# Kernel optimization log

Hardware: AMD Instinct MI355X
Metric: run time of the kernel (lower is better)

Reference implementation:

```python
import jax, jax.numpy as jnp
import numpy as np

B, D_IN, UNITS, KFEAT = 2048, 2048, 1024, 49


def setup_inputs() -> dict:
    key = jax.random.key(0)
    ks = jax.random.split(key, 10)
    s = 0.02  # small init scale to keep sigmoids/tanh unsaturated
    return {
        "inputs": jax.random.normal(ks[0], (B, D_IN), jnp.float32),
        "h_tm": jax.random.normal(ks[1], (B, UNITS), jnp.float32),
        "m_tm": jax.random.normal(ks[2], (B, UNITS), jnp.float32),
        "v_seq": jax.random.normal(ks[3], (B, KFEAT, UNITS), jnp.float32),
        # gate weights stacked along output dim in order [f, i, o, g, a]
        "W_gates": jax.random.normal(ks[4], (UNITS, 5 * UNITS), jnp.float32) * s,
        "U_gates": jax.random.normal(ks[5], (D_IN, 5 * UNITS), jnp.float32) * s,
        "b_gates": jnp.zeros((5 * UNITS,), jnp.float32),
        "W_z": jax.random.normal(ks[6], (UNITS, KFEAT + 1), jnp.float32) * s,
        "U_z": jax.random.normal(ks[7], (UNITS, KFEAT + 1), jnp.float32) * s,
        "W_h": jax.random.normal(ks[8], (KFEAT + 1, 1), jnp.float32) * s,
    }


def reference(inputs, h_tm, m_tm, v_seq, W_gates, U_gates, b_gates, W_z, U_z, W_h):
    U = h_tm.shape[-1]
    # fused gate pre-activations: [B, 5U]
    z = h_tm @ W_gates + inputs @ U_gates + b_gates
    f, i, o, g, a = (z[:, j * U:(j + 1) * U] for j in range(5))
    ft = jax.nn.sigmoid(f)
    it = jax.nn.sigmoid(i)
    ot = jax.nn.sigmoid(o)
    gt = jax.nn.sigmoid(g)
    at = jnp.tanh(a)
    mt = m_tm * ft + it * at               # memory cell
    tanh_mt = jnp.tanh(mt)
    ht = ot * tanh_mt                      # hidden state
    st = gt * tanh_mt                      # visual sentinel
    # sentinel-augmented features: [B, K+1, U]
    v_expand = jnp.concatenate([v_seq, st[:, None, :]], axis=1)
    vtt = jnp.einsum('bku,uz->bkz', v_expand, W_z)   # [B, K+1, K+1]
    dtt = (ht @ U_z)[:, None, :]                     # broadcast over K+1 (K.repeat)
    zt = jnp.einsum('bkz,zo->bko', jnp.tanh(vtt + dtt), W_h)  # [B, K+1, 1]
    # NOTE: original uses keras softmax with default axis=-1 on a size-1 axis
    alpha_t = jax.nn.softmax(zt, axis=-1)            # [B, K+1, 1]
    ct = jnp.sum(alpha_t * v_expand, axis=1)         # batch_dot(axes=1) + squeeze
    return (ht + ct, ht, mt)
```

## Files before the change

kernel.cpp:

```cpp
#include <hip/hip_runtime.h>
#include <stdint.h>

#define BB   2048
#define DIN  2048
#define UU   1024
#define KF   49
#define GM   2048
#define GK   3072
#define GN   5120

typedef __bf16  bf16x8 __attribute__((ext_vector_type(8)));
typedef float   f32x4  __attribute__((ext_vector_type(4)));

static __device__ __forceinline__ unsigned short f2bf(float f) {
    union { float f; unsigned u; } x; x.f = f;
    unsigned u = x.u;
    unsigned r = (u + 0x7fffu + ((u >> 16) & 1u)) >> 16;
    return (unsigned short)r;
}

__global__ void prep(const float* __restrict__ h, const float* __restrict__ x,
                     const float* __restrict__ Wg, const float* __restrict__ Ug,
                     unsigned short* __restrict__ A, unsigned short* __restrict__ Wt) {
    __shared__ float t[32][36];
    if (blockIdx.x < 6144) {
        int idx = blockIdx.x * 256 + threadIdx.x;
        int b = idx / (GK / 4);
        int k = (idx % (GK / 4)) * 4;
        float4 v;
        if (k < UU) v = *(const float4*)(h + (size_t)b * UU + k);
        else        v = *(const float4*)(x + (size_t)b * DIN + (k - UU));
        ushort4 o;
        o.x = f2bf(v.x); o.y = f2bf(v.y); o.z = f2bf(v.z); o.w = f2bf(v.w);
        *(ushort4*)(A + (size_t)idx * 4) = o;
    } else {
        int bid2 = blockIdx.x - 6144;
        int k0 = (bid2 % (GK / 32)) * 32;
        int n0 = (bid2 / (GK / 32)) * 32;
        int r  = threadIdx.x >> 3;
        int cq = threadIdx.x & 7;
        int k = k0 + r;
        const float* src = (k < UU) ? (Wg + (size_t)k * GN) : (Ug + (size_t)(k - UU) * GN);
        *(float4*)&t[r][cq * 4] = *(const float4*)(src + n0 + cq * 4);
        __syncthreads();
        ushort4 o;
        o.x = f2bf(t[cq * 4 + 0][r]);
        o.y = f2bf(t[cq * 4 + 1][r]);
        o.z = f2bf(t[cq * 4 + 2][r]);
        o.w = f2bf(t[cq * 4 + 3][r]);
        *(ushort4*)(Wt + (size_t)(n0 + r) * GK + k0 + cq * 4) = o;
    }
}

__global__ __launch_bounds__(256, 2) void gemm_fused(
        const unsigned short* __restrict__ A, const unsigned short* __restrict__ Wt,
        const float* __restrict__ m_tm, const float* __restrict__ bg,
        const float* __restrict__ v_seq, float* __restrict__ out) {
    __shared__ __align__(16) char lds[18432];

    const int tid  = threadIdx.x;
    const int lane = tid & 63;
    const int wave = tid >> 6;
    const int wr = wave >> 1, wc = wave & 1;
    const int brow  = blockIdx.y * 128;
    const int ucol0 = blockIdx.x * 32;

    f32x4 acc[4][5];
#pragma unroll
    for (int m = 0; m < 4; m++)
#pragma unroll
        for (int g = 0; g < 5; g++) acc[m][g] = (f32x4){0.f, 0.f, 0.f, 0.f};

    const unsigned short* src[5];
    int ldsoff[5];
    bool valid[5];
#pragma unroll
    for (int t = 0; t < 5; t++) {
        int base = t * 256 + wave * 64;
        int j = base + lane;
        valid[t]  = (base < 1152);
        ldsoff[t] = j * 16;
        if (j < 512) {
            src[t] = A + (size_t)(brow + (j >> 2)) * GK + (j & 3) * 8;
        } else {
            int j2 = j - 512;
            int g = j2 >> 7;
            int n = (j2 >> 2) & 31;
            int c = j2 & 3;
            int gg = (g > 4) ? 4 : g;
            src[t] = Wt + ((size_t)gg * UU + ucol0 + n) * GK + c * 8;
        }
    }

    float4 vacc[4];
#pragma unroll
    for (int r = 0; r < 4; r++) vacc[r] = (float4){0.f, 0.f, 0.f, 0.f};
    const float* vp = v_seq + ((size_t)(brow + (tid >> 3)) * KF) * UU + ucol0 + (tid & 7) * 4;

    for (int k0 = 0; k0 < GK; k0 += 32) {
#pragma unroll
        for (int t = 0; t < 5; t++)
            if (valid[t])
                __builtin_amdgcn_global_load_lds(
                    (const __attribute__((address_space(1))) void*)(src[t] + k0),
                    (__attribute__((address_space(3))) void*)(lds + ldsoff[t]), 16, 0, 0);

        {
            const int kk = k0 >> 6;
            const float4 va0 = *(const float4*)(vp + ((size_t)0  * KF + kk) * UU);
            const float4 va1 = *(const float4*)(vp + ((size_t)32 * KF + kk) * UU);
            const float4 vb0 = *(const float4*)(vp + ((size_t)64 * KF + kk) * UU);
            const float4 vb1 = *(const float4*)(vp + ((size_t)96 * KF + kk) * UU);
            if (((k0 >> 5) & 1) == 0) {
                vacc[0].x += va0.x; vacc[0].y += va0.y; vacc[0].z += va0.z; vacc[0].w += va0.w;
                vacc[1].x += va1.x; vacc[1].y += va1.y; vacc[1].z += va1.z; vacc[1].w += va1.w;
            } else {
                vacc[2].x += vb0.x; vacc[2].y += vb0.y; vacc[2].z += vb0.z; vacc[2].w += vb0.w;
                vacc[3].x += vb1.x; vacc[3].y += vb1.y; vacc[3].z += vb1.z; vacc[3].w += vb1.w;
            }
        }

        __syncthreads();

        bf16x8 af[4], bfg[5];
#pragma unroll
        for (int m = 0; m < 4; m++)
            af[m] = *(const bf16x8*)(lds + (wr * 64 + m * 16 + (lane & 15)) * 64 + (lane >> 4) * 16);
#pragma unroll
        for (int g = 0; g < 5; g++)
            bfg[g] = *(const bf16x8*)(lds + 8192 + g * 2048 + (wc * 16 + (lane & 15)) * 64 + (lane >> 4) * 16);
#pragma unroll
        for (int m = 0; m < 4; m++)
#pragma unroll
            for (int g = 0; g < 5; g++)
                acc[m][g] = __builtin_amdgcn_mfma_f32_16x16x32_bf16(af[m], bfg[g], acc[m][g], 0, 0, 0);
        __syncthreads();
    }

#pragma unroll
    for (int r = 0; r < 4; r++) {
        const float4 v = *(const float4*)(vp + ((size_t)(32 * r) * KF + 48) * UU);
        vacc[r].x += v.x; vacc[r].y += v.y; vacc[r].z += v.z; vacc[r].w += v.w;
    }

    float* lv = (float*)lds;
    {
        const int lr = tid >> 3, lc = (tid & 7) * 4;
#pragma unroll
        for (int r = 0; r < 4; r++)
            *(float4*)&lv[(size_t)(lr + 32 * r) * 36 + lc] = vacc[r];
    }
    __syncthreads();

    const int ucol = ucol0 + wc * 16 + (lane & 15);
    const int lcol = wc * 16 + (lane & 15);
    const float b0 = bg[0 * UU + ucol];
    const float b1 = bg[1 * UU + ucol];
    const float b2 = bg[2 * UU + ucol];
    const float b3 = bg[3 * UU + ucol];
    const float b4 = bg[4 * UU + ucol];
    const int r0 = brow + wr * 64 + ((lane >> 4) << 2);
    const int lr0 = wr * 64 + ((lane >> 4) << 2);
    float* out0 = out;
    float* out1 = out + (size_t)GM * UU;
    float* out2 = out + 2 * (size_t)GM * UU;
#pragma unroll
    for (int m = 0; m < 4; m++) {
#pragma unroll
        for (int j = 0; j < 4; j++) {
            const int row = r0 + m * 16 + j;
            const size_t idx = (size_t)row * UU + ucol;
            const float vs  = lv[(size_t)(lr0 + m * 16 + j) * 36 + lcol];
            const float mtm = m_tm[idx];
            const float f = acc[m][0][j] + b0;
            const float i = acc[m][1][j] + b1;
            const float o = acc[m][2][j] + b2;
            const float g = acc[m][3][j] + b3;
            const float a = acc[m][4][j] + b4;
            const float ft = 1.f / (1.f + __expf(-f));
            const float it = 1.f / (1.f + __expf(-i));
            const float ot = 1.f / (1.f + __expf(-o));
            const float gt = 1.f / (1.f + __expf(-g));
            const float at = tanhf(a);
            const float mtv = mtm * ft + it * at;
            const float tm  = tanhf(mtv);
            const float ht  = ot * tm;
            const float st  = gt * tm;
            out0[idx] = ht + vs + st;
            out1[idx] = ht;
            out2[idx] = mtv;
        }
    }
}

extern "C" void kernel_launch(void* const* d_in, const int* in_sizes, int n_in,
                              void* d_out, int out_size, void* d_ws, size_t ws_size,
                              hipStream_t stream) {
    (void)in_sizes; (void)n_in; (void)out_size; (void)ws_size;
    const float* inputs  = (const float*)d_in[0];
    const float* h_tm    = (const float*)d_in[1];
    const float* m_tm    = (const float*)d_in[2];
    const float* v_seq   = (const float*)d_in[3];
    const float* W_gates = (const float*)d_in[4];
    const float* U_gates = (const float*)d_in[5];
    const float* b_gates = (const float*)d_in[6];

    char* ws = (char*)d_ws;
    unsigned short* Abf = (unsigned short*)ws;
    unsigned short* Wt  = (unsigned short*)(ws + 12582912);
    float* out = (float*)d_out;

    hipLaunchKernelGGL(prep, dim3(6144 + (GK / 32) * (GN / 32)), dim3(256), 0, stream,
                       h_tm, inputs, W_gates, U_gates, Abf, Wt);
    hipLaunchKernelGGL(gemm_fused, dim3(UU / 32, GM / 128), dim3(256), 0, stream,
                       Abf, Wt, m_tm, b_gates, v_seq, out);
}
```

Before: 209.3 us.

## Double-buffer LDS staging, widen block to 64 units with 8 waves, interleave gate weights

The fused GEMM kernel now uses 512 threads covering 64 output units per block and double-buffers the LDS tiles, so global-to-LDS loads for the next K step overlap MFMA work on the current one and one barrier per step is dropped. The prep kernel writes the transposed weights with the five gates interleaved per unit, which makes each block's B tile one contiguous slab. The v_seq reduction is re-indexed to the wider tile. In exchange the kernel uses more LDS (56 KB per block), which may reduce occupancy, and halves the number of blocks.

```diff
diff --git a/kernel.cpp b/kernel.cpp
--- a/kernel.cpp
+++ b/kernel.cpp
@@ -8,6 +8,13 @@
 #define GM   2048
 #define GK   3072
 #define GN   5120
+
+#define BM    128
+#define UC    64
+#define BROWS 320
+#define BKS   32
+#define NST   96
+#define BUFB  28672
 
 typedef __bf16  bf16x8 __attribute__((ext_vector_type(8)));
 typedef float   f32x4  __attribute__((ext_vector_type(4)));
@@ -43,27 +50,31 @@
         const float* src = (k < UU) ? (Wg + (size_t)k * GN) : (Ug + (size_t)(k - UU) * GN);
         *(float4*)&t[r][cq * 4] = *(const float4*)(src + n0 + cq * 4);
         __syncthreads();
+        int n = n0 + r;
+        int u = n & (UU - 1);
+        int g = n >> 10;
         ushort4 o;
         o.x = f2bf(t[cq * 4 + 0][r]);
         o.y = f2bf(t[cq * 4 + 1][r]);
         o.z = f2bf(t[cq * 4 + 2][r]);
         o.w = f2bf(t[cq * 4 + 3][r]);
-        *(ushort4*)(Wt + (size_t)(n0 + r) * GK + k0 + cq * 4) = o;
-    }
-}
-
-__global__ __launch_bounds__(256, 2) void gemm_fused(
+        *(ushort4*)(Wt + (size_t)(u * 5 + g) * GK + k0 + cq * 4) = o;
+    }
+}
+
+__global__ __launch_bounds__(512, 2) void gemm_fused(
         const unsigned short* __restrict__ A, const unsigned short* __restrict__ Wt,
         const float* __restrict__ m_tm, const float* __restrict__ bg,
         const float* __restrict__ v_seq, float* __restrict__ out) {
-    __shared__ __align__(16) char lds[18432];
+    __shared__ __align__(16) char lds[2 * 28672];
 
     const int tid  = threadIdx.x;
     const int lane = tid & 63;
     const int wave = tid >> 6;
-    const int wr = wave >> 1, wc = wave & 1;
-    const int brow  = blockIdx.y * 128;
-    const int ucol0 = blockIdx.x * 32;
+    const int wr = wave >> 2;
+    const int wc = wave & 3;
+    const int brow  = blockIdx.y * BM;
+    const int ucol0 = blockIdx.x * UC;
 
     f32x4 acc[4][5];
 #pragma unroll
@@ -71,84 +82,97 @@
 #pragma unroll
         for (int g = 0; g < 5; g++) acc[m][g] = (f32x4){0.f, 0.f, 0.f, 0.f};
 
-    const unsigned short* src[5];
-    int ldsoff[5];
-    bool valid[5];
-#pragma unroll
-    for (int t = 0; t < 5; t++) {
-        int base = t * 256 + wave * 64;
-        int j = base + lane;
-        valid[t]  = (base < 1152);
-        ldsoff[t] = j * 16;
+    const unsigned short* src[4];
+    int ldsoff[4];
+#pragma unroll
+    for (int t = 0; t < 4; t++) {
+        int j = t * 512 + tid;
         if (j < 512) {
             src[t] = A + (size_t)(brow + (j >> 2)) * GK + (j & 3) * 8;
+            ldsoff[t] = j * 16;
         } else {
-            int j2 = j - 512;
-            int g = j2 >> 7;
-            int n = (j2 >> 2) & 31;
-            int c = j2 & 3;
-            int gg = (g > 4) ? 4 : g;
-            src[t] = Wt + ((size_t)gg * UU + ucol0 + n) * GK + c * 8;
-        }
-    }
-
-    float4 vacc[4];
-#pragma unroll
-    for (int r = 0; r < 4; r++) vacc[r] = (float4){0.f, 0.f, 0.f, 0.f};
-    const float* vp = v_seq + ((size_t)(brow + (tid >> 3)) * KF) * UU + ucol0 + (tid & 7) * 4;
-
-    for (int k0 = 0; k0 < GK; k0 += 32) {
-#pragma unroll
-        for (int t = 0; t < 5; t++)
-            if (valid[t])
-                __builtin_amdgcn_global_load_lds(
-                    (const __attribute__((address_space(1))) void*)(src[t] + k0),
-                    (__attribute__((address_space(3))) void*)(lds + ldsoff[t]), 16, 0, 0);
-
+            int jj = j - 512;
+            if (jj > 1279) jj = 1279;
+            src[t] = Wt + (size_t)((size_t)ucol0 * 5 + (jj >> 2)) * GK + (jj & 3) * 8;
+            ldsoff[t] = 8192 + jj * 16;
+        }
+    }
+
+    const int aoff = (wr * 64 + (lane & 15)) * 64 + (lane >> 4) * 16;
+    const int boff = 8192 + ((wc * 16 + (lane & 15)) * 5) * 64 + (lane >> 4) * 16;
+
+    auto STAGE = [&](int kstep, int bufbase) {
+        const int koff = kstep * BKS;
+#pragma unroll
+        for (int t = 0; t < 3; t++)
+            __builtin_amdgcn_global_load_lds(
+                (const __attribute__((address_space(1))) void*)(src[t] + koff),
+                (__attribute__((address_space(3))) void*)(lds + bufbase + ldsoff[t]), 16, 0, 0);
+        if (tid < 256)
+            __builtin_amdgcn_global_load_lds(
+                (const __attribute__((address_space(1))) void*)(src[3] + koff),
+                (__attribute__((address_space(3))) void*)(lds + bufbase + ldsoff[3]), 16, 0, 0);
+    };
+
+    auto COMPUTE = [&](int bufbase) {
+        bf16x8 af[4], bfr[5];
+#pragma unroll
+        for (int m = 0; m < 4; m++) af[m]  = *(const bf16x8*)(lds + bufbase + aoff + m * 1024);
+#pragma unroll
+        for (int g = 0; g < 5; g++) bfr[g] = *(const bf16x8*)(lds + bufbase + boff + g * 64);
+#pragma unroll
+        for (int m = 0; m < 4; m++)
+#pragma unroll
+            for (int g = 0; g < 5; g++)
+                acc[m][g] = __builtin_amdgcn_mfma_f32_16x16x32_bf16(af[m], bfr[g], acc[m][g], 0, 0, 0);
+    };
+
+    const float* vp = v_seq + (size_t)(brow + (tid >> 4)) * (KF * UU) + ucol0 + (tid & 15) * 4;
+    const size_t RG = (size_t)32 * KF * UU;
+    float4 vacc0 = {0,0,0,0}, vacc1 = {0,0,0,0}, vacc2 = {0,0,0,0}, vacc3 = {0,0,0,0};
+
+    STAGE(0, 0);
+    __syncthreads();
+
+    for (int tp = 0; tp < 48; ++tp) {
         {
-            const int kk = k0 >> 6;
-            const float4 va0 = *(const float4*)(vp + ((size_t)0  * KF + kk) * UU);
-            const float4 va1 = *(const float4*)(vp + ((size_t)32 * KF + kk) * UU);
-            const float4 vb0 = *(const float4*)(vp + ((size_t)64 * KF + kk) * UU);
-            const float4 vb1 = *(const float4*)(vp + ((size_t)96 * KF + kk) * UU);
-            if (((k0 >> 5) & 1) == 0) {
-                vacc[0].x += va0.x; vacc[0].y += va0.y; vacc[0].z += va0.z; vacc[0].w += va0.w;
-                vacc[1].x += va1.x; vacc[1].y += va1.y; vacc[1].z += va1.z; vacc[1].w += va1.w;
-            } else {
-                vacc[2].x += vb0.x; vacc[2].y += vb0.y; vacc[2].z += vb0.z; vacc[2].w += vb0.w;
-                vacc[3].x += vb1.x; vacc[3].y += vb1.y; vacc[3].z += vb1.z; vacc[3].w += vb1.w;
-            }
-        }
-
-        __syncthreads();
-
-        bf16x8 af[4], bfg[5];
-#pragma unroll
-        for (int m = 0; m < 4; m++)
-            af[m] = *(const bf16x8*)(lds + (wr * 64 + m * 16 + (lane & 15)) * 64 + (lane >> 4) * 16);
-#pragma unroll
-        for (int g = 0; g < 5; g++)
-            bfg[g] = *(const bf16x8*)(lds + 8192 + g * 2048 + (wc * 16 + (lane & 15)) * 64 + (lane >> 4) * 16);
-#pragma unroll
-        for (int m = 0; m < 4; m++)
-#pragma unroll
-            for (int g = 0; g < 5; g++)
-                acc[m][g] = __builtin_amdgcn_mfma_f32_16x16x32_bf16(af[m], bfg[g], acc[m][g], 0, 0, 0);
-        __syncthreads();
-    }
-
-#pragma unroll
-    for (int r = 0; r < 4; r++) {
-        const float4 v = *(const float4*)(vp + ((size_t)(32 * r) * KF + 48) * UU);
-        vacc[r].x += v.x; vacc[r].y += v.y; vacc[r].z += v.z; vacc[r].w += v.w;
+            STAGE(2 * tp + 1, BUFB);
+            const float4 v0 = *(const float4*)(vp + (size_t)tp * UU);
+            const float4 v1 = *(const float4*)(vp + RG + (size_t)tp * UU);
+            COMPUTE(0);
+            vacc0.x += v0.x; vacc0.y += v0.y; vacc0.z += v0.z; vacc0.w += v0.w;
+            vacc1.x += v1.x; vacc1.y += v1.y; vacc1.z += v1.z; vacc1.w += v1.w;
+            __syncthreads();
+        }
+        {
+            if (tp < 47) STAGE(2 * tp + 2, 0);
+            const float4 v2 = *(const float4*)(vp + 2 * RG + (size_t)tp * UU);
+            const float4 v3 = *(const float4*)(vp + 3 * RG + (size_t)tp * UU);
+            COMPUTE(BUFB);
+            vacc2.x += v2.x; vacc2.y += v2.y; vacc2.z += v2.z; vacc2.w += v2.w;
+            vacc3.x += v3.x; vacc3.y += v3.y; vacc3.z += v3.z; vacc3.w += v3.w;
+            __syncthreads();
+        }
+    }
+
+    {
+        const float4 w0 = *(const float4*)(vp + (size_t)48 * UU);
+        const float4 w1 = *(const float4*)(vp + RG + (size_t)48 * UU);
+        const float4 w2 = *(const float4*)(vp + 2 * RG + (size_t)48 * UU);
+        const float4 w3 = *(const float4*)(vp + 3 * RG + (size_t)48 * UU);
+        vacc0.x += w0.x; vacc0.y += w0.y; vacc0.z += w0.z; vacc0.w += w0.w;
+        vacc1.x += w1.x; vacc1.y += w1.y; vacc1.z += w1.z; vacc1.w += w1.w;
+        vacc2.x += w2.x; vacc2.y += w2.y; vacc2.z += w2.z; vacc2.w += w2.w;
+        vacc3.x += w3.x; vacc3.y += w3.y; vacc3.z += w3.z; vacc3.w += w3.w;
     }
 
     float* lv = (float*)lds;
     {
-        const int lr = tid >> 3, lc = (tid & 7) * 4;
-#pragma unroll
-        for (int r = 0; r < 4; r++)
-            *(float4*)&lv[(size_t)(lr + 32 * r) * 36 + lc] = vacc[r];
+        const int xr = tid >> 4, xc = (tid & 15) * 4;
+        *(float4*)&lv[(size_t)(xr +  0) * 68 + xc] = vacc0;
+        *(float4*)&lv[(size_t)(xr + 32) * 68 + xc] = vacc1;
+        *(float4*)&lv[(size_t)(xr + 64) * 68 + xc] = vacc2;
+        *(float4*)&lv[(size_t)(xr + 96) * 68 + xc] = vacc3;
     }
     __syncthreads();
 
@@ -159,7 +183,6 @@
     const float b2 = bg[2 * UU + ucol];
     const float b3 = bg[3 * UU + ucol];
     const float b4 = bg[4 * UU + ucol];
-    const int r0 = brow + wr * 64 + ((lane >> 4) << 2);
     const int lr0 = wr * 64 + ((lane >> 4) << 2);
     float* out0 = out;
     float* out1 = out + (size_t)GM * UU;
@@ -168,9 +191,10 @@
     for (int m = 0; m < 4; m++) {
 #pragma unroll
         for (int j = 0; j < 4; j++) {
-            const int row = r0 + m * 16 + j;
+            const int lrow = lr0 + m * 16 + j;
+            const int row  = brow + lrow;
             const size_t idx = (size_t)row * UU + ucol;
-            const float vs  = lv[(size_t)(lr0 + m * 16 + j) * 36 + lcol];
+            const float vs  = lv[(size_t)lrow * 68 + lcol];
             const float mtm = m_tm[idx];
             const float f = acc[m][0][j] + b0;
             const float i = acc[m][1][j] + b1;
@@ -212,6 +236,6 @@
 
     hipLaunchKernelGGL(prep, dim3(6144 + (GK / 32) * (GN / 32)), dim3(256), 0, stream,
                        h_tm, inputs, W_gates, U_gates, Abf, Wt);
-    hipLaunchKernelGGL(gemm_fused, dim3(UU / 32, GM / 128), dim3(256), 0, stream,
+    hipLaunchKernelGGL(gemm_fused, dim3(UU / UC, GM / BM), dim3(512), 0, stream,
                        Abf, Wt, m_tm, b_gates, v_seq, out);
 }
```

After: 194.9 us. 1.07x faster.

## Triple-buffer GEMM LDS stages with async prefetch and swizzled block mapping

Applied to the files above, without the earlier changes.

Replaces the single-buffer load/sync/compute loop with a three-stage LDS ring. Global-to-LDS loads for step k+2 are issued before computing step k, and completion is tracked with explicit vmcnt waits and a single barrier per step. The v_seq reduction loads move to inline-asm prefetches one step ahead, and block indices are swizzled for better L2 locality across blocks. LDS per block triples, which may limit occupancy, and the hand-counted vmcnt values must match the number of outstanding loads.

```diff
diff --git a/kernel.cpp b/kernel.cpp
--- a/kernel.cpp
+++ b/kernel.cpp
@@ -9,8 +9,14 @@
 #define GK   3072
 #define GN   5120
 
+#define BKS  32
+#define SZB  18432
+
 typedef __bf16  bf16x8 __attribute__((ext_vector_type(8)));
 typedef float   f32x4  __attribute__((ext_vector_type(4)));
+
+#define VL(dst, ptr) asm volatile("global_load_dwordx4 %0, %1, off" \
+                                  : "=v"(dst) : "v"(ptr) : "memory")
 
 static __device__ __forceinline__ unsigned short f2bf(float f) {
     union { float f; unsigned u; } x; x.f = f;
@@ -56,14 +62,15 @@
         const unsigned short* __restrict__ A, const unsigned short* __restrict__ Wt,
         const float* __restrict__ m_tm, const float* __restrict__ bg,
         const float* __restrict__ v_seq, float* __restrict__ out) {
-    __shared__ __align__(16) char lds[18432];
+    __shared__ __align__(16) char lds[3 * SZB];
 
     const int tid  = threadIdx.x;
     const int lane = tid & 63;
     const int wave = tid >> 6;
     const int wr = wave >> 1, wc = wave & 1;
-    const int brow  = blockIdx.y * 128;
-    const int ucol0 = blockIdx.x * 32;
+    const int swz = (blockIdx.x & 7) * 64 + (blockIdx.x >> 3);
+    const int brow  = (swz >> 5) * 128;
+    const int ucol0 = (swz & 31) * 32;
 
     f32x4 acc[4][5];
 #pragma unroll
@@ -73,82 +80,116 @@
 
     const unsigned short* src[5];
     int ldsoff[5];
-    bool valid[5];
-#pragma unroll
-    for (int t = 0; t < 5; t++) {
-        int base = t * 256 + wave * 64;
-        int j = base + lane;
-        valid[t]  = (base < 1152);
-        ldsoff[t] = j * 16;
-        if (j < 512) {
-            src[t] = A + (size_t)(brow + (j >> 2)) * GK + (j & 3) * 8;
+#pragma unroll
+    for (int r = 0; r < 5; ++r) {
+        if (r < 2) {
+            int j = r * 256 + tid;
+            src[r] = A + (size_t)(brow + (j >> 2)) * GK + (j & 3) * 8;
+            ldsoff[r] = j * 16;
         } else {
-            int j2 = j - 512;
+            int j2 = (r < 4) ? (r - 2) * 256 + tid : 512 + (tid & 127);
             int g = j2 >> 7;
-            int n = (j2 >> 2) & 31;
+            int nn = (j2 >> 2) & 31;
             int c = j2 & 3;
-            int gg = (g > 4) ? 4 : g;
-            src[t] = Wt + ((size_t)gg * UU + ucol0 + n) * GK + c * 8;
-        }
-    }
-
-    float4 vacc[4];
-#pragma unroll
-    for (int r = 0; r < 4; r++) vacc[r] = (float4){0.f, 0.f, 0.f, 0.f};
-    const float* vp = v_seq + ((size_t)(brow + (tid >> 3)) * KF) * UU + ucol0 + (tid & 7) * 4;
-
-    for (int k0 = 0; k0 < GK; k0 += 32) {
-#pragma unroll
-        for (int t = 0; t < 5; t++)
-            if (valid[t])
-                __builtin_amdgcn_global_load_lds(
-                    (const __attribute__((address_space(1))) void*)(src[t] + k0),
-                    (__attribute__((address_space(3))) void*)(lds + ldsoff[t]), 16, 0, 0);
-
+            src[r] = Wt + ((size_t)g * UU + ucol0 + nn) * GK + c * 8;
+            ldsoff[r] = 8192 + j2 * 16;
+        }
+    }
+
+    int aoff[4], boff[5];
+#pragma unroll
+    for (int m = 0; m < 4; m++)
+        aoff[m] = (wr * 64 + m * 16 + (lane & 15)) * 64 + (lane >> 4) * 16;
+#pragma unroll
+    for (int g = 0; g < 5; g++)
+        boff[g] = 8192 + (g * 32 + wc * 16 + (lane & 15)) * 64 + (lane >> 4) * 16;
+
+    auto STAGE = [&](int kstep, int bufb) {
+        const int ko = kstep * BKS;
+#pragma unroll
+        for (int r = 0; r < 5; ++r)
+            __builtin_amdgcn_global_load_lds(
+                (const __attribute__((address_space(1))) void*)(src[r] + ko),
+                (__attribute__((address_space(3))) void*)(lds + bufb + ldsoff[r]), 16, 0, 0);
+    };
+    auto COMPUTE = [&](int bufb) {
+        bf16x8 af[4], bfr[5];
+#pragma unroll
+        for (int m = 0; m < 4; m++) af[m]  = *(const bf16x8*)(lds + bufb + aoff[m]);
+#pragma unroll
+        for (int g = 0; g < 5; g++) bfr[g] = *(const bf16x8*)(lds + bufb + boff[g]);
+#pragma unroll
+        for (int m = 0; m < 4; m++)
+#pragma unroll
+            for (int g = 0; g < 5; g++)
+                acc[m][g] = __builtin_amdgcn_mfma_f32_16x16x32_bf16(af[m], bfr[g], acc[m][g], 0, 0, 0);
+    };
+
+    const float* vpa = v_seq + (size_t)(brow + (tid >> 2)) * (KF * UU) + ucol0 + (tid & 3) * 4;
+    const float* vpc = vpa + (size_t)64 * KF * UU;
+    f32x4 sa = {0,0,0,0}, sb = {0,0,0,0}, sc = {0,0,0,0}, sd = {0,0,0,0};
+    f32x4 XA, XB, YA, YB;
+
+    STAGE(0, 0);
+    VL(XA, vpa);
+    VL(XB, vpa + 16);
+    STAGE(1, SZB);
+    VL(YA, vpc);
+    VL(YB, vpc + 16);
+    asm volatile("s_waitcnt vmcnt(7)" ::: "memory");
+    __builtin_amdgcn_s_barrier();
+    __builtin_amdgcn_sched_barrier(0);
+
+    int cb = 0;
+    for (int tp = 0; tp < 47; ++tp) {
         {
-            const int kk = k0 >> 6;
-            const float4 va0 = *(const float4*)(vp + ((size_t)0  * KF + kk) * UU);
-            const float4 va1 = *(const float4*)(vp + ((size_t)32 * KF + kk) * UU);
-            const float4 vb0 = *(const float4*)(vp + ((size_t)64 * KF + kk) * UU);
-            const float4 vb1 = *(const float4*)(vp + ((size_t)96 * KF + kk) * UU);
-            if (((k0 >> 5) & 1) == 0) {
-                vacc[0].x += va0.x; vacc[0].y += va0.y; vacc[0].z += va0.z; vacc[0].w += va0.w;
-                vacc[1].x += va1.x; vacc[1].y += va1.y; vacc[1].z += va1.z; vacc[1].w += va1.w;
-            } else {
-                vacc[2].x += vb0.x; vacc[2].y += vb0.y; vacc[2].z += vb0.z; vacc[2].w += vb0.w;
-                vacc[3].x += vb1.x; vacc[3].y += vb1.y; vacc[3].z += vb1.z; vacc[3].w += vb1.w;
-            }
-        }
-
-        __syncthreads();
-
-        bf16x8 af[4], bfg[5];
-#pragma unroll
-        for (int m = 0; m < 4; m++)
-            af[m] = *(const bf16x8*)(lds + (wr * 64 + m * 16 + (lane & 15)) * 64 + (lane >> 4) * 16);
-#pragma unroll
-        for (int g = 0; g < 5; g++)
-            bfg[g] = *(const bf16x8*)(lds + 8192 + g * 2048 + (wc * 16 + (lane & 15)) * 64 + (lane >> 4) * 16);
-#pragma unroll
-        for (int m = 0; m < 4; m++)
-#pragma unroll
-            for (int g = 0; g < 5; g++)
-                acc[m][g] = __builtin_amdgcn_mfma_f32_16x16x32_bf16(af[m], bfg[g], acc[m][g], 0, 0, 0);
-        __syncthreads();
-    }
-
-#pragma unroll
-    for (int r = 0; r < 4; r++) {
-        const float4 v = *(const float4*)(vp + ((size_t)(32 * r) * KF + 48) * UU);
-        vacc[r].x += v.x; vacc[r].y += v.y; vacc[r].z += v.z; vacc[r].w += v.w;
+            sa += XA; sb += XB;
+            int sbuf = cb + 2 * SZB; if (sbuf >= 3 * SZB) sbuf -= 3 * SZB;
+            STAGE(2 * tp + 2, sbuf);
+            VL(XA, vpa + (size_t)(tp + 1) * UU);
+            VL(XB, vpa + (size_t)(tp + 1) * UU + 16);
+            COMPUTE(cb);
+            asm volatile("s_waitcnt vmcnt(7)" ::: "memory");
+            __builtin_amdgcn_s_barrier();
+            __builtin_amdgcn_sched_barrier(0);
+            cb += SZB; if (cb >= 3 * SZB) cb = 0;
+        }
+        {
+            sc += YA; sd += YB;
+            int sbuf = cb + 2 * SZB; if (sbuf >= 3 * SZB) sbuf -= 3 * SZB;
+            STAGE(2 * tp + 3, sbuf);
+            VL(YA, vpc + (size_t)(tp + 1) * UU);
+            VL(YB, vpc + (size_t)(tp + 1) * UU + 16);
+            COMPUTE(cb);
+            asm volatile("s_waitcnt vmcnt(7)" ::: "memory");
+            __builtin_amdgcn_s_barrier();
+            __builtin_amdgcn_sched_barrier(0);
+            cb += SZB; if (cb >= 3 * SZB) cb = 0;
+        }
+    }
+    sa += XA; sb += XB;
+    COMPUTE(cb);
+    asm volatile("s_waitcnt vmcnt(0)" ::: "memory");
+    __builtin_amdgcn_s_barrier();
+    __builtin_amdgcn_sched_barrier(0);
+    cb += SZB; if (cb >= 3 * SZB) cb = 0;
+    sc += YA; sd += YB;
+    COMPUTE(cb);
+
+    {
+        sa += *(const f32x4*)(vpa + (size_t)48 * UU);
+        sb += *(const f32x4*)(vpa + (size_t)48 * UU + 16);
+        sc += *(const f32x4*)(vpc + (size_t)48 * UU);
+        sd += *(const f32x4*)(vpc + (size_t)48 * UU + 16);
     }
 
     float* lv = (float*)lds;
     {
-        const int lr = tid >> 3, lc = (tid & 7) * 4;
-#pragma unroll
-        for (int r = 0; r < 4; r++)
-            *(float4*)&lv[(size_t)(lr + 32 * r) * 36 + lc] = vacc[r];
+        const int r = tid >> 2, c1 = (tid & 3) * 4;
+        *(f32x4*)&lv[(size_t)r * 36 + c1]             = sa;
+        *(f32x4*)&lv[(size_t)r * 36 + c1 + 16]        = sb;
+        *(f32x4*)&lv[(size_t)(r + 64) * 36 + c1]      = sc;
+        *(f32x4*)&lv[(size_t)(r + 64) * 36 + c1 + 16] = sd;
     }
     __syncthreads();
 
@@ -159,7 +200,6 @@
     const float b2 = bg[2 * UU + ucol];
     const float b3 = bg[3 * UU + ucol];
     const float b4 = bg[4 * UU + ucol];
-    const int r0 = brow + wr * 64 + ((lane >> 4) << 2);
     const int lr0 = wr * 64 + ((lane >> 4) << 2);
     float* out0 = out;
     float* out1 = out + (size_t)GM * UU;
@@ -168,9 +208,10 @@
     for (int m = 0; m < 4; m++) {
 #pragma unroll
         for (int j = 0; j < 4; j++) {
-            const int row = r0 + m * 16 + j;
+            const int lrow = lr0 + m * 16 + j;
+            const int row  = brow + lrow;
             const size_t idx = (size_t)row * UU + ucol;
-            const float vs  = lv[(size_t)(lr0 + m * 16 + j) * 36 + lcol];
+            const float vs  = lv[(size_t)lrow * 36 + lcol];
             const float mtm = m_tm[idx];
             const float f = acc[m][0][j] + b0;
             const float i = acc[m][1][j] + b1;
@@ -212,6 +253,6 @@
 
     hipLaunchKernelGGL(prep, dim3(6144 + (GK / 32) * (GN / 32)), dim3(256), 0, stream,
                        h_tm, inputs, W_gates, U_gates, Abf, Wt);
-    hipLaunchKernelGGL(gemm_fused, dim3(UU / 32, GM / 128), dim3(256), 0, stream,
+    hipLaunchKernelGGL(gemm_fused, dim3(512), dim3(256), 0, stream,
                        Abf, Wt, m_tm, b_gates, v_seq, out);
 }
```

New measurement: 217.3 us. 1.04x slower.
